# Optimization experiments

Hardware: AMD Instinct MI355X
Metric: run time of the kernel (lower is better)

Reference implementation:

```python
import jax, jax.numpy as jnp
import numpy as np
import math

HEAD_DIM = 64
N_HEADS = 64
N_KV = 8
HIDDEN = 2880
BASE = 150000.0
INIT_CTX = 4096
SCALING = 32.0
NTK_ALPHA = 1.0
NTK_BETA = 32.0
SM_SCALE = 1.0 / math.sqrt(HEAD_DIM)
EPS = 1e-5


def _rope_cos_sin(T):
    # YaRN-scaled rotary frequencies (see RotaryEmbedding._compute_concentration_and_inv_freq)
    freq = BASE ** (jnp.arange(0, HEAD_DIM, 2, dtype=jnp.float32) / HEAD_DIM)
    concentration = 0.1 * math.log(SCALING) + 1.0
    d_half = HEAD_DIM / 2
    low = d_half * math.log(INIT_CTX / (NTK_BETA * 2 * math.pi)) / math.log(BASE)
    high = d_half * math.log(INIT_CTX / (NTK_ALPHA * 2 * math.pi)) / math.log(BASE)
    interp = 1.0 / (SCALING * freq)
    extrap = 1.0 / freq
    ramp = (jnp.arange(d_half, dtype=jnp.float32) - low) / (high - low)
    mask = 1.0 - jnp.clip(ramp, 0.0, 1.0)
    inv_freq = interp * (1.0 - mask) + extrap * mask
    tpos = jnp.arange(T, dtype=jnp.float32)
    freqs = jnp.outer(tpos, inv_freq)            # [T, HEAD_DIM/2]
    return jnp.cos(freqs) * concentration, jnp.sin(freqs) * concentration


def _apply_rotary(x, cos, sin):
    # x: [T, H, D]; cos/sin: [T, D/2]
    cos = cos[:, None, :]
    sin = sin[:, None, :]
    x1, x2 = jnp.split(x, 2, axis=-1)
    return jnp.concatenate([x1 * cos - x2 * sin, x2 * cos + x1 * sin], axis=-1)


def setup_inputs() -> dict:
    key = jax.random.key(0)
    ks = jax.random.split(key, 4)
    T = 2048
    qkv_dim = HEAD_DIM * (N_HEADS + 2 * N_KV)   # 4608
    x = jax.random.normal(ks[0], (T, HIDDEN), jnp.float32)
    norm_scale = jnp.ones((HIDDEN,), jnp.float32)
    qkv_w = jax.random.normal(ks[1], (qkv_dim, HIDDEN), jnp.float32) * 0.02
    qkv_b = jnp.zeros((qkv_dim,), jnp.float32)
    out_w = jax.random.normal(ks[2], (HIDDEN, N_HEADS * HEAD_DIM), jnp.float32) * 0.02
    out_b = jnp.zeros((HIDDEN,), jnp.float32)
    return {"x": x, "norm_scale": norm_scale, "qkv_w": qkv_w, "qkv_b": qkv_b,
            "out_w": out_w, "out_b": out_b}


def reference(x, norm_scale, qkv_w, qkv_b, out_w, out_b):
    T = x.shape[0]
    # RMSNorm (computed in fp32, as in the torch module)
    t = x * jax.lax.rsqrt(jnp.mean(x * x, axis=-1, keepdims=True) + EPS) * norm_scale
    # Fused QKV projection
    qkv = t @ qkv_w.T + qkv_b                    # [T, 4608]
    qd = N_HEADS * HEAD_DIM
    kd = N_KV * HEAD_DIM
    q = qkv[:, :qd].reshape(T, N_HEADS, HEAD_DIM)
    k = qkv[:, qd:qd + kd].reshape(T, N_KV, HEAD_DIM)
    v = qkv[:, qd + kd:qd + 2 * kd].reshape(T, N_KV, HEAD_DIM)
    # YaRN RoPE
    cos, sin = _rope_cos_sin(T)
    q = _apply_rotary(q, cos, sin)
    k = _apply_rotary(k, cos, sin)
    # GQA causal attention (cache=None path: sinks ignored, full causal mask)
    qmult = N_HEADS // N_KV
    q = q.reshape(T, N_KV, qmult, HEAD_DIM)      # [T, g, m, d]
    scores = jnp.einsum('qgmd,kgd->gmqk', q, k) * SM_SCALE  # [g, m, T, T]
    causal = jnp.arange(T)[:, None] >= jnp.arange(T)[None, :]
    scores = jnp.where(causal[None, None], scores, -jnp.inf)
    attn = jax.nn.softmax(scores, axis=-1)
    o = jnp.einsum('gmqk,kgd->qgmd', attn, v).reshape(T, N_HEADS * HEAD_DIM)
    # Output projection + residual
    return o @ out_w.T + out_b + x
```

## Files before the change

### kernel.cpp

```cpp
#include <hip/hip_runtime.h>
#include <stdint.h>
#include <math.h>

#define T_SEQ 2048
#define HID   2880
#define QKV_D 5120
#define OD    4096
#define NQH   64
#define SM_SCALE 0.125f
#define LOG2E 1.44269504088896340736f
#define SSL (SM_SCALE * LOG2E)

typedef float f32x4 __attribute__((ext_vector_type(4)));
typedef float f32x16 __attribute__((ext_vector_type(16)));
typedef short bf16x8 __attribute__((ext_vector_type(8)));

__device__ __forceinline__ unsigned short f2bf(float f) {
  union { float f; unsigned u; } v; v.f = f;
  unsigned r = v.u + 0x7fffu + ((v.u >> 16) & 1u);
  return (unsigned short)(r >> 16);
}
__device__ __forceinline__ float bf2f(unsigned short h) {
  union { unsigned u; float f; } v; v.u = ((unsigned)h) << 16;
  return v.f;
}
__device__ __forceinline__ void gld_lds16(const void* g, void* l) {
  __builtin_amdgcn_global_load_lds(
      (const __attribute__((address_space(1))) unsigned int*)g,
      (__attribute__((address_space(3))) unsigned int*)l, 16, 0, 0);
}

__global__ __launch_bounds__(256) void rmsnorm_k(const float* __restrict__ x,
                                                 const float* __restrict__ scale,
                                                 unsigned short* __restrict__ t) {
  int row = blockIdx.x;
  const float4* xr = (const float4*)(x + (size_t)row * HID);
  float s = 0.f;
  for (int i = threadIdx.x; i < 720; i += 256) {
    float4 a = xr[i];
    s += a.x * a.x + a.y * a.y + a.z * a.z + a.w * a.w;
  }
#pragma unroll
  for (int off = 32; off; off >>= 1) s += __shfl_down(s, off);
  __shared__ float wsum[4];
  int w = threadIdx.x >> 6, lane = threadIdx.x & 63;
  if (lane == 0) wsum[w] = s;
  __syncthreads();
  float tot = wsum[0] + wsum[1] + wsum[2] + wsum[3];
  float r = rsqrtf(tot / (float)HID + 1e-5f);
  const float4* sc4 = (const float4*)scale;
  ushort4* tr = (ushort4*)(t + (size_t)row * HID);
  for (int i = threadIdx.x; i < 720; i += 256) {
    float4 a = xr[i]; float4 b = sc4[i];
    ushort4 o;
    o.x = f2bf(a.x * r * b.x); o.y = f2bf(a.y * r * b.y);
    o.z = f2bf(a.z * r * b.z); o.w = f2bf(a.w * r * b.w);
    tr[i] = o;
  }
}

__global__ __launch_bounds__(256) void f2bf_k(const float* __restrict__ in,
                                              unsigned short* __restrict__ out, int n4) {
  int i = blockIdx.x * 256 + threadIdx.x;
  int stride = gridDim.x * 256;
  for (; i < n4; i += stride) {
    float4 a = ((const float4*)in)[i];
    ushort4 o;
    o.x = f2bf(a.x); o.y = f2bf(a.y); o.z = f2bf(a.z); o.w = f2bf(a.w);
    ((ushort4*)out)[i] = o;
  }
}

__global__ __launch_bounds__(256) void rope_tab_k(float* __restrict__ ct, float* __restrict__ st) {
  int idx = blockIdx.x * 256 + threadIdx.x;
  int i = idx & 31, t = idx >> 5;
  double fi = (double)i;
  double freq = pow(150000.0, fi / 32.0);
  double lb = log(150000.0);
  double low  = 32.0 * log(4096.0 / (32.0 * 2.0 * M_PI)) / lb;
  double high = 32.0 * log(4096.0 / (1.0  * 2.0 * M_PI)) / lb;
  double interp = 1.0 / (32.0 * freq);
  double extrap = 1.0 / freq;
  double ramp = (fi - low) / (high - low);
  ramp = fmin(fmax(ramp, 0.0), 1.0);
  double mask = 1.0 - ramp;
  double invf = interp * (1.0 - mask) + extrap * mask;
  double conc = 0.1 * log(32.0) + 1.0;
  double th = (double)t * invf;
  ct[idx] = (float)(cos(th) * conc);
  st[idx] = (float)(sin(th) * conc);
}

__global__ __launch_bounds__(256) void rope_apply_k(unsigned short* __restrict__ qkv,
                                                    const float* __restrict__ ct,
                                                    const float* __restrict__ st) {
  int idx = blockIdx.x * 256 + threadIdx.x;
  int i = idx & 31;
  int hh = (idx >> 5) % 72;
  int t = idx / (72 * 32);
  size_t base = (size_t)t * QKV_D + hh * 64 + i;
  float x1 = bf2f(qkv[base]), x2 = bf2f(qkv[base + 32]);
  float c = ct[t * 32 + i], s = st[t * 32 + i];
  qkv[base]      = f2bf(x1 * c - x2 * s);
  qkv[base + 32] = f2bf(x2 * c + x1 * s);
}

__global__ __launch_bounds__(256) void vtrans_k(const unsigned short* __restrict__ qkv,
                                                unsigned short* __restrict__ vt) {
  __shared__ unsigned short tile[64][72];
  int g = blockIdx.y;
  int t0 = blockIdx.x * 64;
  int tid = threadIdx.x;
#pragma unroll
  for (int p = 0; p < 2; ++p) {
    int ch = p * 256 + tid;
    int i = ch >> 3, j0 = (ch & 7) * 8;
    bf16x8 v = *(const bf16x8*)(qkv + (size_t)(t0 + i) * QKV_D + 4608 + g * 64 + j0);
    *(bf16x8*)&tile[i][j0] = v;
  }
  __syncthreads();
#pragma unroll
  for (int p = 0; p < 2; ++p) {
    int ch = p * 256 + tid;
    int j = ch >> 3, i0 = (ch & 7) * 8;
    union { unsigned short u[8]; bf16x8 v; } pk;
#pragma unroll
    for (int m = 0; m < 8; ++m) pk.u[m] = tile[i0 + m][j];
    *(bf16x8*)(vt + (size_t)(g * 64 + j) * T_SEQ + t0 + i0) = pk.v;
  }
}

template <bool FINAL>
__global__ __launch_bounds__(256) void gemm_k(const unsigned short* __restrict__ A,
                                              const unsigned short* __restrict__ B,
                                              const float* __restrict__ bias,
                                              const float* __restrict__ resid,
                                              unsigned short* __restrict__ Cb,
                                              float* __restrict__ Cf,
                                              int M, int N, int K) {
  __shared__ unsigned short As[128 * 32];
  __shared__ unsigned short Bs[128 * 32];
  int tid = threadIdx.x;
  int w = tid >> 6, lane = tid & 63;
  int g = lane >> 4, ln = lane & 15;
  int m0 = blockIdx.y * 128, n0 = blockIdx.x * 128;
  int wr = w >> 1, wc = w & 1;
  f32x4 acc[4][4];
#pragma unroll
  for (int a = 0; a < 4; a++)
#pragma unroll
    for (int b = 0; b < 4; b++) acc[a][b] = (f32x4){0.f, 0.f, 0.f, 0.f};

  int chunk0 = w * 64 + lane;
  for (int k0 = 0; k0 < K; k0 += 32) {
#pragma unroll
    for (int p = 0; p < 2; ++p) {
      int ch = p * 256 + chunk0;
      int row = ch >> 2, cc = ch & 3;
      int gch = cc ^ (row & 3);
      gld_lds16(A + (size_t)(m0 + row) * K + k0 + gch * 8, &As[(p * 256 + w * 64) * 8]);
      int rowB = n0 + row; if (rowB > N - 1) rowB = N - 1;
      gld_lds16(B + (size_t)rowB * K + k0 + gch * 8, &Bs[(p * 256 + w * 64) * 8]);
    }
    __syncthreads();
    bf16x8 af[4], bfr[4];
#pragma unroll
    for (int mi = 0; mi < 4; ++mi) {
      int rm = wr * 64 + mi * 16 + ln;
      int c = g ^ (rm & 3);
      af[mi] = *(const bf16x8*)&As[rm * 32 + c * 8];
    }
#pragma unroll
    for (int ni = 0; ni < 4; ++ni) {
      int rn = wc * 64 + ni * 16 + ln;
      int c = g ^ (rn & 3);
      bfr[ni] = *(const bf16x8*)&Bs[rn * 32 + c * 8];
    }
#pragma unroll
    for (int mi = 0; mi < 4; ++mi)
#pragma unroll
      for (int ni = 0; ni < 4; ++ni)
        acc[mi][ni] = __builtin_amdgcn_mfma_f32_16x16x32_bf16(af[mi], bfr[ni], acc[mi][ni], 0, 0, 0);
    __syncthreads();
  }
#pragma unroll
  for (int mi = 0; mi < 4; ++mi)
#pragma unroll
    for (int ni = 0; ni < 4; ++ni) {
      int colB = n0 + wc * 64 + ni * 16 + ln;
      if (colB >= N) continue;
      float bv = bias[colB];
#pragma unroll
      for (int r = 0; r < 4; ++r) {
        int rowC = m0 + wr * 64 + mi * 16 + g * 4 + r;
        float v = acc[mi][ni][r] + bv;
        if (FINAL) {
          Cf[(size_t)rowC * N + colB] = v + resid[(size_t)rowC * N + colB];
        } else {
          Cb[(size_t)rowC * N + colB] = f2bf(v);
        }
      }
    }
}

__global__ __launch_bounds__(256) void attn2_k(const unsigned short* __restrict__ qkv,
                                               const unsigned short* __restrict__ vt,
                                               unsigned short* __restrict__ o) {
  __shared__ unsigned short Ks[2][64 * 64];
  __shared__ unsigned short Vs[2][64 * 64];
  int h = blockIdx.x;
  int qt = (int)gridDim.y - 1 - (int)blockIdx.y;
  int tid = threadIdx.x;
  int w = tid >> 6, lane = tid & 63;
  int l31 = lane & 31, hi = lane >> 5;
  int qb0 = qt * 128;
  int q0w = qb0 + w * 32;
  int kvh = h >> 3;
  const unsigned short* kbase = qkv + 4096 + (size_t)kvh * 64;
  const unsigned short* vtb = vt + (size_t)kvh * 64 * T_SEQ;

  bf16x8 qf[4];
  {
    const unsigned short* qrow = qkv + (size_t)(q0w + l31) * QKV_D + h * 64;
#pragma unroll
    for (int dt = 0; dt < 4; ++dt)
      qf[dt] = *(const bf16x8*)(qrow + dt * 16 + hi * 8);
  }
  f32x16 oacc[2];
#pragma unroll
  for (int r = 0; r < 16; ++r) { oacc[0][r] = 0.f; oacc[1][r] = 0.f; }
  float m_run = -1e30f, l_run = 0.f;
  int nt = qt * 2 + 2;

  auto STAGE = [&](int t, int buf) {
    int kv0 = t * 64;
#pragma unroll
    for (int p = 0; p < 2; ++p) {
      int ch = p * 256 + w * 64 + lane;
      int row = ch >> 3, cc = ch & 7;
      int gch = cc ^ (row & 7);
      gld_lds16(kbase + (size_t)(kv0 + row) * QKV_D + gch * 8, &Ks[buf][(p * 256 + w * 64) * 8]);
      gld_lds16(vtb + (size_t)row * T_SEQ + kv0 + gch * 8, &Vs[buf][(p * 256 + w * 64) * 8]);
    }
  };

  STAGE(0, 0);
  __syncthreads();
  for (int t = 0; t < nt; ++t) {
    int cur = t & 1;
    if (t + 1 < nt) STAGE(t + 1, cur ^ 1);
    int kv0 = t * 64;
    if (kv0 <= q0w + 31) {
      const unsigned short* K_ = Ks[cur];
      const unsigned short* V_ = Vs[cur];
      f32x16 pa[2];
#pragma unroll
      for (int kt2 = 0; kt2 < 2; ++kt2) {
        f32x16 acc;
#pragma unroll
        for (int r = 0; r < 16; ++r) acc[r] = 0.f;
        int rk = kt2 * 32 + l31;
#pragma unroll
        for (int dt = 0; dt < 4; ++dt) {
          int c = dt * 2 + hi;
          bf16x8 kf = *(const bf16x8*)&K_[rk * 64 + (c ^ (rk & 7)) * 8];
          acc = __builtin_amdgcn_mfma_f32_32x32x16_bf16(kf, qf[dt], acc, 0, 0, 0);
        }
        pa[kt2] = acc;
      }
      bool diag = (kv0 + 64 > q0w);
      int q = q0w + l31;
      float s2[32];
#pragma unroll
      for (int kt2 = 0; kt2 < 2; ++kt2)
#pragma unroll
        for (int r = 0; r < 16; ++r) {
          float x = pa[kt2][r] * SSL;
          if (diag) {
            int k = kv0 + kt2 * 32 + (r & 3) + 8 * (r >> 2) + 4 * hi;
            if (k > q) x = -3.0e38f;
          }
          s2[kt2 * 16 + r] = x;
        }
      float mx = s2[0];
#pragma unroll
      for (int i = 1; i < 32; ++i) mx = fmaxf(mx, s2[i]);
      mx = fmaxf(mx, __shfl_xor(mx, 32));
      float mnew = fmaxf(m_run, mx);
      float alpha = exp2f(m_run - mnew);
      m_run = mnew;
      float sum = 0.f;
#pragma unroll
      for (int i = 0; i < 32; ++i) {
        float p = exp2f(s2[i] - mnew);
        s2[i] = p;
        sum += p;
      }
      sum += __shfl_xor(sum, 32);
      l_run = l_run * alpha + sum;
#pragma unroll
      for (int r = 0; r < 16; ++r) { oacc[0][r] *= alpha; oacc[1][r] *= alpha; }
      unsigned pw[16];
#pragma unroll
      for (int kt2 = 0; kt2 < 2; ++kt2)
#pragma unroll
        for (int i = 0; i < 8; ++i) {
          unsigned r_;
          asm("v_cvt_pk_bf16_f32 %0, %1, %2"
              : "=v"(r_) : "v"(s2[kt2 * 16 + 2 * i]), "v"(s2[kt2 * 16 + 2 * i + 1]));
          pw[kt2 * 8 + i] = r_;
        }
      unsigned bw[2][2][4];
#pragma unroll
      for (int kt2 = 0; kt2 < 2; ++kt2)
#pragma unroll
        for (int a = 0; a < 2; ++a) {
          unsigned p0 = pw[kt2 * 8 + a * 4 + 0];
          unsigned p1 = pw[kt2 * 8 + a * 4 + 1];
          unsigned p2 = pw[kt2 * 8 + a * 4 + 2];
          unsigned p3 = pw[kt2 * 8 + a * 4 + 3];
          unsigned e0 = (unsigned)__shfl_xor((int)p0, 32);
          unsigned e1 = (unsigned)__shfl_xor((int)p1, 32);
          unsigned e2 = (unsigned)__shfl_xor((int)p2, 32);
          unsigned e3 = (unsigned)__shfl_xor((int)p3, 32);
          bw[kt2][a][0] = hi ? e2 : p0;
          bw[kt2][a][1] = hi ? e3 : p1;
          bw[kt2][a][2] = hi ? p2 : e0;
          bw[kt2][a][3] = hi ? p3 : e1;
        }
#pragma unroll
      for (int db = 0; db < 2; ++db) {
        f32x16 acc = oacc[db];
        int rd = db * 32 + l31;
#pragma unroll
        for (int kt2 = 0; kt2 < 2; ++kt2)
#pragma unroll
          for (int a = 0; a < 2; ++a) {
            int c = kt2 * 4 + a * 2 + hi;
            bf16x8 vf = *(const bf16x8*)&V_[rd * 64 + (c ^ (rd & 7)) * 8];
            union { unsigned u[4]; bf16x8 v; } pun;
            pun.u[0] = bw[kt2][a][0]; pun.u[1] = bw[kt2][a][1];
            pun.u[2] = bw[kt2][a][2]; pun.u[3] = bw[kt2][a][3];
            acc = __builtin_amdgcn_mfma_f32_32x32x16_bf16(vf, pun.v, acc, 0, 0, 0);
          }
        oacc[db] = acc;
      }
    }
    __syncthreads();
  }
  float inv = 1.f / l_run;
  int q = q0w + l31;
#pragma unroll
  for (int db = 0; db < 2; ++db)
#pragma unroll
    for (int r = 0; r < 16; r += 2) {
      int d = db * 32 + (r & 3) + 8 * (r >> 2) + 4 * hi;
      unsigned short lo_ = f2bf(oacc[db][r] * inv);
      unsigned short hi_ = f2bf(oacc[db][r + 1] * inv);
      unsigned u = (unsigned)lo_ | ((unsigned)hi_ << 16);
      *(unsigned*)(o + (size_t)q * OD + h * 64 + d) = u;
    }
}

extern "C" void kernel_launch(void* const* d_in, const int* in_sizes, int n_in,
                              void* d_out, int out_size, void* d_ws, size_t ws_size,
                              hipStream_t stream) {
  const float* x          = (const float*)d_in[0];
  const float* norm_scale = (const float*)d_in[1];
  const float* qkv_w      = (const float*)d_in[2];
  const float* qkv_b      = (const float*)d_in[3];
  const float* out_w      = (const float*)d_in[4];
  const float* out_b      = (const float*)d_in[5];
  float* out = (float*)d_out;

  char* ws = (char*)d_ws;
  size_t off = 0;
  auto alloc = [&](size_t bytes) {
    void* p = ws + off;
    off += (bytes + 255) & ~(size_t)255;
    return p;
  };
  unsigned short* t_bf = (unsigned short*)alloc((size_t)T_SEQ * HID * 2);
  unsigned short* wqkv = (unsigned short*)alloc((size_t)QKV_D * HID * 2);
  unsigned short* wout = (unsigned short*)alloc((size_t)HID * OD * 2);
  unsigned short* qkv  = (unsigned short*)alloc((size_t)T_SEQ * QKV_D * 2);
  unsigned short* obuf = (unsigned short*)alloc((size_t)T_SEQ * OD * 2);
  unsigned short* vtb  = (unsigned short*)alloc((size_t)8 * 64 * T_SEQ * 2);
  float* ct = (float*)alloc((size_t)T_SEQ * 32 * 4);
  float* st = (float*)alloc((size_t)T_SEQ * 32 * 4);

  rmsnorm_k<<<dim3(T_SEQ), dim3(256), 0, stream>>>(x, norm_scale, t_bf);
  f2bf_k<<<dim3(1024), dim3(256), 0, stream>>>(qkv_w, wqkv, QKV_D * HID / 4);
  f2bf_k<<<dim3(1024), dim3(256), 0, stream>>>(out_w, wout, HID * OD / 4);
  rope_tab_k<<<dim3(T_SEQ * 32 / 256), dim3(256), 0, stream>>>(ct, st);
  gemm_k<false><<<dim3(QKV_D / 128, T_SEQ / 128), dim3(256), 0, stream>>>(
      t_bf, wqkv, qkv_b, nullptr, qkv, nullptr, T_SEQ, QKV_D, HID);
  rope_apply_k<<<dim3(T_SEQ * 72 * 32 / 256), dim3(256), 0, stream>>>(qkv, ct, st);
  vtrans_k<<<dim3(T_SEQ / 64, 8), dim3(256), 0, stream>>>(qkv, vtb);
  attn2_k<<<dim3(NQH, T_SEQ / 128), dim3(256), 0, stream>>>(qkv, vtb, obuf);
  gemm_k<true><<<dim3((HID + 127) / 128, T_SEQ / 128), dim3(256), 0, stream>>>(
      obuf, wout, out_b, x, nullptr, out, T_SEQ, HID, OD);
}
```

Measured before the change: 455.9 us.

## Double-buffer GEMM LDS tiles with 8 waves and swizzled block order

Rewrites the GEMM kernel to use 512 threads (8 waves) per 128x128 tile, with each wave computing a 32x64 sub-tile. The LDS tiles are double-buffered so the next K-slice loads while the current one runs through MFMA, leaving one barrier per iteration. A workgroup-index swizzle remaps block order, likely to improve L2 reuse across concurrently running blocks. This trades per-wave arithmetic intensity for more waves and latency hiding, and doubles LDS use per block.

```diff
diff --git a/kernel.cpp b/kernel.cpp
--- a/kernel.cpp
+++ b/kernel.cpp
@@ -131,60 +131,70 @@
 }
 
 template <bool FINAL>
-__global__ __launch_bounds__(256) void gemm_k(const unsigned short* __restrict__ A,
-                                              const unsigned short* __restrict__ B,
-                                              const float* __restrict__ bias,
-                                              const float* __restrict__ resid,
-                                              unsigned short* __restrict__ Cb,
-                                              float* __restrict__ Cf,
-                                              int M, int N, int K) {
-  __shared__ unsigned short As[128 * 32];
-  __shared__ unsigned short Bs[128 * 32];
+__global__ __launch_bounds__(512, 4) void gemm8_k(const unsigned short* __restrict__ A,
+                                                  const unsigned short* __restrict__ B,
+                                                  const float* __restrict__ bias,
+                                                  const float* __restrict__ resid,
+                                                  unsigned short* __restrict__ Cb,
+                                                  float* __restrict__ Cf,
+                                                  int M, int N, int K) {
+  __shared__ unsigned short As[2][128 * 32];
+  __shared__ unsigned short Bs[2][128 * 32];
   int tid = threadIdx.x;
   int w = tid >> 6, lane = tid & 63;
   int g = lane >> 4, ln = lane & 15;
-  int m0 = blockIdx.y * 128, n0 = blockIdx.x * 128;
+  int nwg = gridDim.x * gridDim.y;
+  int lin = blockIdx.y * gridDim.x + blockIdx.x;
+  int swz = (lin & 7) * (nwg >> 3) + (lin >> 3);
+  int bx = swz % gridDim.x, by = swz / gridDim.x;
+  int m0 = by * 128, n0 = bx * 128;
   int wr = w >> 1, wc = w & 1;
-  f32x4 acc[4][4];
-#pragma unroll
-  for (int a = 0; a < 4; a++)
+  f32x4 acc[2][4];
+#pragma unroll
+  for (int a = 0; a < 2; a++)
 #pragma unroll
     for (int b = 0; b < 4; b++) acc[a][b] = (f32x4){0.f, 0.f, 0.f, 0.f};
 
-  int chunk0 = w * 64 + lane;
-  for (int k0 = 0; k0 < K; k0 += 32) {
-#pragma unroll
-    for (int p = 0; p < 2; ++p) {
-      int ch = p * 256 + chunk0;
-      int row = ch >> 2, cc = ch & 3;
-      int gch = cc ^ (row & 3);
-      gld_lds16(A + (size_t)(m0 + row) * K + k0 + gch * 8, &As[(p * 256 + w * 64) * 8]);
-      int rowB = n0 + row; if (rowB > N - 1) rowB = N - 1;
-      gld_lds16(B + (size_t)rowB * K + k0 + gch * 8, &Bs[(p * 256 + w * 64) * 8]);
-    }
-    __syncthreads();
-    bf16x8 af[4], bfr[4];
-#pragma unroll
-    for (int mi = 0; mi < 4; ++mi) {
-      int rm = wr * 64 + mi * 16 + ln;
+  int srow = tid >> 2, scc = tid & 3;
+  int sg = scc ^ (srow & 3);
+  const unsigned short* gA = A + (size_t)(m0 + srow) * K + sg * 8;
+  int rowB = n0 + srow; if (rowB > N - 1) rowB = N - 1;
+  const unsigned short* gB = B + (size_t)rowB * K + sg * 8;
+
+  int nt = K >> 5;
+  gld_lds16(gA, &As[0][(w * 64) * 8]);
+  gld_lds16(gB, &Bs[0][(w * 64) * 8]);
+  __syncthreads();
+  int cur = 0;
+  for (int t = 0; t < nt; ++t) {
+    if (t + 1 < nt) {
+      int k0 = (t + 1) << 5;
+      gld_lds16(gA + k0, &As[cur ^ 1][(w * 64) * 8]);
+      gld_lds16(gB + k0, &Bs[cur ^ 1][(w * 64) * 8]);
+    }
+    bf16x8 af[2], bfr[4];
+#pragma unroll
+    for (int mi = 0; mi < 2; ++mi) {
+      int rm = wr * 32 + mi * 16 + ln;
       int c = g ^ (rm & 3);
-      af[mi] = *(const bf16x8*)&As[rm * 32 + c * 8];
+      af[mi] = *(const bf16x8*)&As[cur][rm * 32 + c * 8];
     }
 #pragma unroll
     for (int ni = 0; ni < 4; ++ni) {
       int rn = wc * 64 + ni * 16 + ln;
       int c = g ^ (rn & 3);
-      bfr[ni] = *(const bf16x8*)&Bs[rn * 32 + c * 8];
-    }
-#pragma unroll
-    for (int mi = 0; mi < 4; ++mi)
+      bfr[ni] = *(const bf16x8*)&Bs[cur][rn * 32 + c * 8];
+    }
+#pragma unroll
+    for (int mi = 0; mi < 2; ++mi)
 #pragma unroll
       for (int ni = 0; ni < 4; ++ni)
         acc[mi][ni] = __builtin_amdgcn_mfma_f32_16x16x32_bf16(af[mi], bfr[ni], acc[mi][ni], 0, 0, 0);
     __syncthreads();
-  }
-#pragma unroll
-  for (int mi = 0; mi < 4; ++mi)
+    cur ^= 1;
+  }
+#pragma unroll
+  for (int mi = 0; mi < 2; ++mi)
 #pragma unroll
     for (int ni = 0; ni < 4; ++ni) {
       int colB = n0 + wc * 64 + ni * 16 + ln;
@@ -192,7 +202,7 @@
       float bv = bias[colB];
 #pragma unroll
       for (int r = 0; r < 4; ++r) {
-        int rowC = m0 + wr * 64 + mi * 16 + g * 4 + r;
+        int rowC = m0 + wr * 32 + mi * 16 + g * 4 + r;
         float v = acc[mi][ni][r] + bv;
         if (FINAL) {
           Cf[(size_t)rowC * N + colB] = v + resid[(size_t)rowC * N + colB];
@@ -393,11 +403,11 @@
   f2bf_k<<<dim3(1024), dim3(256), 0, stream>>>(qkv_w, wqkv, QKV_D * HID / 4);
   f2bf_k<<<dim3(1024), dim3(256), 0, stream>>>(out_w, wout, HID * OD / 4);
   rope_tab_k<<<dim3(T_SEQ * 32 / 256), dim3(256), 0, stream>>>(ct, st);
-  gemm_k<false><<<dim3(QKV_D / 128, T_SEQ / 128), dim3(256), 0, stream>>>(
+  gemm8_k<false><<<dim3(QKV_D / 128, T_SEQ / 128), dim3(512), 0, stream>>>(
       t_bf, wqkv, qkv_b, nullptr, qkv, nullptr, T_SEQ, QKV_D, HID);
   rope_apply_k<<<dim3(T_SEQ * 72 * 32 / 256), dim3(256), 0, stream>>>(qkv, ct, st);
   vtrans_k<<<dim3(T_SEQ / 64, 8), dim3(256), 0, stream>>>(qkv, vtb);
   attn2_k<<<dim3(NQH, T_SEQ / 128), dim3(256), 0, stream>>>(qkv, vtb, obuf);
-  gemm_k<true><<<dim3((HID + 127) / 128, T_SEQ / 128), dim3(256), 0, stream>>>(
+  gemm8_k<true><<<dim3((HID + 127) / 128, T_SEQ / 128), dim3(512), 0, stream>>>(
       obuf, wout, out_b, x, nullptr, out, T_SEQ, HID, OD);
 }
```

Result: faster. 426.8 us (-6.4%).
